# Kernel tuning notes

Hardware: AMD Instinct MI355X
Metric: run time of the kernel (lower is better)

The kernel has to match this reference:

```python
import jax, jax.numpy as jnp
import numpy as np

B, S, D, H = 4, 8192, 512, 8
HD = D // H  # head_dim = 64


def setup_inputs() -> dict:
    key0 = jax.random.key(0)
    ks = jax.random.split(key0, 8)
    scale_in = (2.0 / (D + 3 * D)) ** 0.5  # xavier_uniform-ish std
    scale_out = (2.0 / (D + D)) ** 0.5
    return {
        "query": jax.random.normal(ks[0], (B, S, D), dtype=jnp.float32),
        "key": jax.random.normal(ks[1], (B, S, D), dtype=jnp.float32),
        "value": jax.random.normal(ks[2], (B, S, D), dtype=jnp.float32),
        "key_padding_mask": jax.random.bernoulli(ks[3], 0.1, (B, S)),  # True = ignore
        "in_proj_weight": jax.random.normal(ks[4], (3 * D, D), dtype=jnp.float32) * scale_in,
        "in_proj_bias": jnp.zeros((3 * D,), dtype=jnp.float32),
        "out_proj_weight": jax.random.normal(ks[5], (D, D), dtype=jnp.float32) * scale_out,
        "out_proj_bias": jnp.zeros((D,), dtype=jnp.float32),
    }


def _phi(x):
    # ELU+1 feature map (strictly positive)
    return jax.nn.elu(x) + 1.0


def reference(query, key, value, key_padding_mask, in_proj_weight, in_proj_bias,
              out_proj_weight, out_proj_bias):
    # NB: the torch module projects q,k,v all from `query`; key/value args are unused.
    qkv = query @ in_proj_weight.T + in_proj_bias  # (B,S,3D)
    q, k, v = jnp.split(qkv, 3, axis=-1)
    # (B,S,D) -> (B,H,S,HD)
    def to_heads(x):
        return x.reshape(B, S, H, HD).transpose(0, 2, 1, 3)
    q = _phi(to_heads(q))
    k = _phi(to_heads(k))
    v = to_heads(v)
    mask = (~key_padding_mask).astype(q.dtype)[:, None, :, None]  # (B,1,S,1)
    k = k * mask
    v = v * mask
    kv = jnp.einsum('bhsd,bhse->bhde', k, v)          # (B,H,HD,HD)
    numerator = jnp.einsum('bhsd,bhde->bhse', q, kv)  # (B,H,S,HD)
    k_sum = k.sum(axis=2)                              # (B,H,HD)
    denominator = jnp.einsum('bhsd,bhd->bhs', q, k_sum)[..., None]
    denominator = jnp.maximum(denominator, 1e-6)
    attn_out = (numerator / denominator).transpose(0, 2, 1, 3).reshape(B, S, D)
    return attn_out @ out_proj_weight.T + out_proj_bias
```

## Files before the change

kernel.cpp:

```cpp
#include <hip/hip_runtime.h>
#include <cstddef>

#define B_   4
#define S_   8192
#define D_   512
#define H_   8
#define HD_  64
#define NROW (B_ * S_)
#define NQ   ((size_t)NROW * D_)

typedef __attribute__((ext_vector_type(4))) float  f32x4;
typedef __attribute__((ext_vector_type(8))) short  s16x8;
typedef __attribute__((ext_vector_type(4))) unsigned short u16x4;
typedef __attribute__((ext_vector_type(8))) unsigned short u16x8;

__device__ __forceinline__ float phi_f(float x) {
    return x > 0.0f ? x + 1.0f : expf(x);
}
__device__ __forceinline__ float bf2f(unsigned short u) {
    return __uint_as_float(((unsigned int)u) << 16);
}
__device__ __forceinline__ unsigned short f2bf(float f) {
    unsigned int u = __float_as_uint(f);
    u += 0x7fffu + ((u >> 16) & 1u);
    return (unsigned short)(u >> 16);
}

#define GLOBAL_AS(p) ((const __attribute__((address_space(1))) void*)(p))
#define LDS_AS(p)    ((__attribute__((address_space(3))) void*)(p))

__global__ void detect_mask(const unsigned char* __restrict__ m, int* __restrict__ flag) {
    __shared__ int sany;
    if (threadIdx.x == 0) sany = 0;
    __syncthreads();
    const uint4* mw = (const uint4*)m;
    unsigned int any = 0;
    #pragma unroll
    for (int r = 0; r < 8; ++r) {
        const uint4 w = mw[r * 256 + threadIdx.x];
        any |= (w.x | w.y | w.z | w.w) & 0xFFFFFF00u;
    }
    if (any) atomicOr(&sany, 1);
    __syncthreads();
    if (threadIdx.x == 0) *flag = sany ? 1 : 0;
}

__global__ __launch_bounds__(256) void convert_all(
    const float* __restrict__ q,  unsigned short* __restrict__ qb,
    const float* __restrict__ wi, unsigned short* __restrict__ wib,
    const float* __restrict__ wo, unsigned short* __restrict__ wob,
    const unsigned char* __restrict__ kpm, const int* __restrict__ flag,
    float* __restrict__ fmask)
{
    const size_t i = (size_t)blockIdx.x * 256 + threadIdx.x;
    {
        const float4 v = *(const float4*)&q[i * 4];
        u16x4 o; o.x = f2bf(v.x); o.y = f2bf(v.y); o.z = f2bf(v.z); o.w = f2bf(v.w);
        *(u16x4*)&qb[i * 4] = o;
    }
    if (i < 786432 / 4) {
        const float4 v = *(const float4*)&wi[i * 4];
        u16x4 o; o.x = f2bf(v.x); o.y = f2bf(v.y); o.z = f2bf(v.z); o.w = f2bf(v.w);
        *(u16x4*)&wib[i * 4] = o;
    }
    if (i < 262144 / 4) {
        const float4 v = *(const float4*)&wo[i * 4];
        u16x4 o; o.x = f2bf(v.x); o.y = f2bf(v.y); o.z = f2bf(v.z); o.w = f2bf(v.w);
        *(u16x4*)&wob[i * 4] = o;
    }
    if (i < NROW) {
        const bool ignore = (*flag) ? (kpm[i] != 0) : (((const int*)kpm)[i] != 0);
        fmask[i] = ignore ? 0.0f : 1.0f;
    }
}

__global__ __launch_bounds__(256) void gemm_mfma(
    const unsigned short* __restrict__ A,  int lda,
    const unsigned short* __restrict__ Bw, int ldb,
    const float* __restrict__ bias, int K, int mode,
    const float* __restrict__ fmask,
    unsigned short* __restrict__ Cq,
    unsigned short* __restrict__ Ck,
    unsigned short* __restrict__ Cv,
    float* __restrict__ Cout)
{
    __shared__ __align__(16) unsigned short As[3][128 * 32];
    __shared__ __align__(16) unsigned short Bs[3][128 * 32];
    __shared__ float fm[128];

    const int t    = threadIdx.x;
    const int lane = t & 63;
    const int wave = t >> 6;
    const int wm   = wave & 1;
    const int wn   = wave >> 1;

    const int nbx = gridDim.x;
    const int nwg = nbx * gridDim.y;
    int id = blockIdx.y * nbx + blockIdx.x;
    id = (id & 7) * (nwg >> 3) + (id >> 3);
    const int m0 = (id / nbx) * 128;
    const int n0 = (id % nbx) * 128;

    if (mode == 0 && t < 128) fm[t] = fmask[m0 + t];

    f32x4 acc[4][4] = {};

    const int sr  = lane >> 2;
    const int skc = (((lane & 3) ^ ((lane >> 3) & 3))) * 8;

    const int nt = K >> 5;

    #define STAGE(kt_, buf_)                                                            \
        do {                                                                            \
            const int k0_ = (kt_) << 5;                                                 \
            _Pragma("unroll")                                                           \
            for (int j = 0; j < 2; ++j) {                                               \
                const int row = wave * 32 + j * 16;                                     \
                const unsigned short* g = A + (size_t)(m0 + row + sr) * lda + k0_ + skc;\
                __builtin_amdgcn_global_load_lds(GLOBAL_AS(g),                          \
                    LDS_AS(&As[(buf_)][row * 32]), 16, 0, 0);                           \
            }                                                                           \
            _Pragma("unroll")                                                           \
            for (int j = 0; j < 2; ++j) {                                               \
                const int row = wave * 32 + j * 16;                                     \
                const unsigned short* g = Bw + (size_t)(n0 + row + sr) * ldb + k0_ + skc;\
                __builtin_amdgcn_global_load_lds(GLOBAL_AS(g),                          \
                    LDS_AS(&Bs[(buf_)][row * 32]), 16, 0, 0);                           \
            }                                                                           \
        } while (0)

    STAGE(0, 0);
    STAGE(1, 1);

    const int fr = lane & 15;
    const int cn = lane >> 4;
    const int fo = (cn ^ ((fr >> 1) & 3)) * 8;

    int cur = 0;
    for (int kt = 0; kt < nt; ++kt) {
        if (kt + 1 < nt) asm volatile("s_waitcnt vmcnt(4)" ::: "memory");
        else             asm volatile("s_waitcnt vmcnt(0)" ::: "memory");
        __builtin_amdgcn_s_barrier();

        if (kt + 2 < nt) {
            int nb = cur + 2; if (nb >= 3) nb -= 3;
            STAGE(kt + 2, nb);
        }

        s16x8 af[4], bf[4];
        #pragma unroll
        for (int i = 0; i < 4; ++i)
            af[i] = *(const s16x8*)&As[cur][(wm * 64 + i * 16 + fr) * 32 + fo];
        #pragma unroll
        for (int j = 0; j < 4; ++j)
            bf[j] = *(const s16x8*)&Bs[cur][(wn * 64 + j * 16 + fr) * 32 + fo];
        #pragma unroll
        for (int i = 0; i < 4; ++i)
            #pragma unroll
            for (int j = 0; j < 4; ++j)
                acc[i][j] = __builtin_amdgcn_mfma_f32_16x16x32_bf16(af[i], bf[j], acc[i][j], 0, 0, 0);

        if (++cur == 3) cur = 0;
    }
    #undef STAGE

    const int col  = lane & 15;
    const int rowq = (lane >> 4) * 4;
    float bj[4];
    #pragma unroll
    for (int j = 0; j < 4; ++j) bj[j] = bias[n0 + wn * 64 + j * 16 + col];

    if (mode == 1) {
        #pragma unroll
        for (int i = 0; i < 4; ++i)
            #pragma unroll
            for (int r = 0; r < 4; ++r) {
                const int m = m0 + wm * 64 + i * 16 + rowq + r;
                #pragma unroll
                for (int j = 0; j < 4; ++j) {
                    const int n = n0 + wn * 64 + j * 16 + col;
                    Cout[(size_t)m * D_ + n] = acc[i][j][r] + bj[j];
                }
            }
    } else {
        const int region = n0 >> 9;
        unsigned short* Cb = region == 0 ? Cq : (region == 1 ? Ck : Cv);
        #pragma unroll
        for (int i = 0; i < 4; ++i)
            #pragma unroll
            for (int r = 0; r < 4; ++r) {
                const int ml = wm * 64 + i * 16 + rowq + r;
                const int m  = m0 + ml;
                const float mk = fm[ml];
                #pragma unroll
                for (int j = 0; j < 4; ++j) {
                    const int n  = (n0 & 511) + wn * 64 + j * 16 + col;
                    float v = acc[i][j][r] + bj[j];
                    if (region == 0)      v = phi_f(v);
                    else if (region == 1) v = phi_f(v) * mk;
                    else                  v = v * mk;
                    Cb[(size_t)m * D_ + n] = f2bf(v);
                }
            }
    }
}

__global__ __launch_bounds__(256) void kv_reduce(
    const unsigned short* __restrict__ kbuf,
    const unsigned short* __restrict__ vbuf,
    float* __restrict__ part_kv,
    float* __restrict__ part_ks)
{
    const int bh = blockIdx.x, chunk = blockIdx.y;
    const int b = bh >> 3, h = bh & 7;

    __shared__ __align__(16) float Ks[16][68];
    __shared__ __align__(16) float Vs[16][68];

    const int t    = threadIdx.x;
    const int wave = t >> 6;
    const int lane = t & 63;
    const int tx   = lane & 7;
    const int ty   = lane >> 3;

    const int sr = (t & 127) >> 3;
    const int sc = (t & 7) * 8;
    const unsigned short* src = (t < 128 ? kbuf : vbuf) + (size_t)b * S_ * D_ + h * HD_;
    float (*dst)[68] = (t < 128) ? Ks : Vs;

    float acc[8][8] = {};
    float ks[8] = {};
    const int s0 = chunk * (S_ / 16);
    const int NIT = 32;

    u16x8 x = *(const u16x8*)&src[(size_t)(s0 + sr) * D_ + sc];

    for (int it = 0; it < NIT; ++it) {
        __syncthreads();
        float4 f0, f1;
        f0.x = bf2f(x[0]); f0.y = bf2f(x[1]); f0.z = bf2f(x[2]); f0.w = bf2f(x[3]);
        f1.x = bf2f(x[4]); f1.y = bf2f(x[5]); f1.z = bf2f(x[6]); f1.w = bf2f(x[7]);
        *(float4*)&dst[sr][sc]     = f0;
        *(float4*)&dst[sr][sc + 4] = f1;
        __syncthreads();
        u16x8 xn = {};
        if (it + 1 < NIT)
            xn = *(const u16x8*)&src[(size_t)(s0 + (it + 1) * 16 + sr) * D_ + sc];
        #pragma unroll
        for (int ss0 = 0; ss0 < 4; ++ss0) {
            const int ss = wave + ss0 * 4;
            const float4 a0 = *(const float4*)&Ks[ss][ty * 8];
            const float4 a1 = *(const float4*)&Ks[ss][ty * 8 + 4];
            const float4 v0 = *(const float4*)&Vs[ss][tx * 8];
            const float4 v1 = *(const float4*)&Vs[ss][tx * 8 + 4];
            const float av[8] = {a0.x, a0.y, a0.z, a0.w, a1.x, a1.y, a1.z, a1.w};
            const float vv[8] = {v0.x, v0.y, v0.z, v0.w, v1.x, v1.y, v1.z, v1.w};
            #pragma unroll
            for (int i2 = 0; i2 < 8; ++i2)
                #pragma unroll
                for (int j2 = 0; j2 < 8; ++j2)
                    acc[i2][j2] += av[i2] * vv[j2];
            if (tx == 0) {
                #pragma unroll
                for (int i2 = 0; i2 < 8; ++i2) ks[i2] += av[i2];
            }
        }
        x = xn;
    }

    const int p = bh * 64 + chunk * 4 + wave;
    float* pk = part_kv + (size_t)p * 4096;
    #pragma unroll
    for (int i2 = 0; i2 < 8; ++i2) {
        #pragma unroll
        for (int j4 = 0; j4 < 2; ++j4) {
            float4 o;
            o.x = acc[i2][j4 * 4 + 0]; o.y = acc[i2][j4 * 4 + 1];
            o.z = acc[i2][j4 * 4 + 2]; o.w = acc[i2][j4 * 4 + 3];
            *(float4*)&pk[(ty * 8 + i2) * 64 + tx * 8 + j4 * 4] = o;
        }
    }
    if (tx == 0) {
        float* ps = part_ks + (size_t)p * 64;
        #pragma unroll
        for (int i2 = 0; i2 < 8; ++i2) ps[ty * 8 + i2] = ks[i2];
    }
}

__global__ void kv_reduce2(const float* __restrict__ part_kv,
                           const float* __restrict__ part_ks,
                           unsigned short* __restrict__ kvT,
                           unsigned short* __restrict__ ksumb)
{
    const int i = blockIdx.x * 256 + threadIdx.x;
    if (i < 32 * 4096) {
        const int bh = i >> 12, de = i & 4095;
        const int d = de >> 6, e = de & 63;
        float s = 0.0f;
        #pragma unroll
        for (int c = 0; c < 64; ++c) s += part_kv[(size_t)(bh * 64 + c) * 4096 + de];
        kvT[bh * 4096 + e * 64 + d] = f2bf(s);
    }
    if (i < 32 * 64) {
        const int bh = i >> 6, e = i & 63;
        float s = 0.0f;
        #pragma unroll
        for (int c = 0; c < 64; ++c) s += part_ks[(size_t)(bh * 64 + c) * 64 + e];
        ksumb[i] = f2bf(s);
    }
}

__global__ __launch_bounds__(256) void apply_attn_mfma(
    const unsigned short* __restrict__ qphi,
    const unsigned short* __restrict__ kvT,
    const unsigned short* __restrict__ ksumb,
    unsigned short* __restrict__ attnb)
{
    const int bh = blockIdx.x;
    const int b  = bh >> 3, h = bh & 7;
    const int m0 = blockIdx.y * 128;

    const int t    = threadIdx.x;
    const int lane = t & 63;
    const int wave = t >> 6;
    const int fr   = lane & 15;
    const int fk   = (lane >> 4) * 8;
    const int row0 = m0 + wave * 32;

    const unsigned short* Ah = qphi + (size_t)(b * S_ + row0) * D_ + h * HD_;
    const unsigned short* Bh = kvT + bh * 4096;
    const unsigned short* Kh = ksumb + bh * 64;

    s16x8 af[2][2], bfr[2][4], bd[2];
    #pragma unroll
    for (int kc = 0; kc < 2; ++kc) {
        #pragma unroll
        for (int i = 0; i < 2; ++i)
            af[kc][i] = *(const s16x8*)&Ah[(size_t)(i * 16 + fr) * D_ + kc * 32 + fk];
        #pragma unroll
        for (int j = 0; j < 4; ++j)
            bfr[kc][j] = *(const s16x8*)&Bh[(j * 16 + fr) * 64 + kc * 32 + fk];
        bd[kc] = *(const s16x8*)&Kh[kc * 32 + fk];
    }

    f32x4 acc[2][4] = {};
    f32x4 accd[2] = {};
    #pragma unroll
    for (int kc = 0; kc < 2; ++kc)
        #pragma unroll
        for (int i = 0; i < 2; ++i) {
            #pragma unroll
            for (int j = 0; j < 4; ++j)
                acc[i][j] = __builtin_amdgcn_mfma_f32_16x16x32_bf16(af[kc][i], bfr[kc][j], acc[i][j], 0, 0, 0);
            accd[i] = __builtin_amdgcn_mfma_f32_16x16x32_bf16(af[kc][i], bd[kc], accd[i], 0, 0, 0);
        }

    const int rq = (lane >> 4) * 4;
    #pragma unroll
    for (int i = 0; i < 2; ++i)
        #pragma unroll
        for (int r = 0; r < 4; ++r) {
            const float inv = 1.0f / fmaxf(accd[i][r], 1e-6f);
            const size_t row = (size_t)(b * S_ + row0 + i * 16 + rq + r);
            #pragma unroll
            for (int j = 0; j < 4; ++j)
                attnb[row * D_ + h * HD_ + j * 16 + fr] = f2bf(acc[i][j][r] * inv);
        }
}

extern "C" void kernel_launch(void* const* d_in, const int* in_sizes, int n_in,
                              void* d_out, int out_size, void* d_ws, size_t ws_size,
                              hipStream_t stream)
{
    const float* query       = (const float*)d_in[0];
    const unsigned char* kpm = (const unsigned char*)d_in[3];
    const float* w_in        = (const float*)d_in[4];
    const float* b_in        = (const float*)d_in[5];
    const float* w_out       = (const float*)d_in[6];
    const float* b_out       = (const float*)d_in[7];
    float* out = (float*)d_out;

    unsigned short* qb    = (unsigned short*)d_ws;
    unsigned short* qphi  = qb    + NQ;
    unsigned short* kpb   = qphi  + NQ;
    unsigned short* vmb   = kpb   + NQ;
    unsigned short* wib   = vmb   + NQ;
    unsigned short* wob   = wib   + 1536 * 512;
    float* fmask   = (float*)(wob + 512 * 512);
    float* part_kv = fmask + NROW;
    float* part_ks = part_kv + (size_t)2048 * 4096;
    unsigned short* kvTb  = (unsigned short*)(part_ks + 2048 * 64);
    unsigned short* ksumb = kvTb + 32 * 4096;
    int*   flag    = (int*)(ksumb + 32 * 64);

    hipLaunchKernelGGL(detect_mask, dim3(1), dim3(256), 0, stream, kpm, flag);
    hipLaunchKernelGGL(convert_all, dim3(16384), dim3(256), 0, stream,
                       query, qb, w_in, wib, w_out, wob, kpm, flag, fmask);

    hipLaunchKernelGGL(gemm_mfma, dim3(1536 / 128, NROW / 128), dim3(256), 0, stream,
                       qb, D_, wib, D_, b_in, D_, 0, fmask,
                       qphi, kpb, vmb, (float*)nullptr);

    hipLaunchKernelGGL(kv_reduce, dim3(32, 16), dim3(256), 0, stream, kpb, vmb, part_kv, part_ks);
    hipLaunchKernelGGL(kv_reduce2, dim3(512), dim3(256), 0, stream,
                       part_kv, part_ks, kvTb, ksumb);

    hipLaunchKernelGGL(apply_attn_mfma, dim3(32, S_ / 128), dim3(256), 0, stream,
                       qphi, kvTb, ksumb, qb);

    hipLaunchKernelGGL(gemm_mfma, dim3(512 / 128, NROW / 128), dim3(256), 0, stream,
                       qb, D_, wob, D_, b_out, D_, 1, (const float*)nullptr,
                       (unsigned short*)nullptr, (unsigned short*)nullptr,
                       (unsigned short*)nullptr, out);
}
```

Baseline: 386.1 us.

## Enlarge GEMM tile to 256x128 and switch to double-buffered LDS pipeline

The shared MFMA GEMM kernel now computes a 256x128 output tile per workgroup. Each wave owns 64 rows across all 128 columns, so it issues 32 MFMAs per k-step against 8 shared B fragments. The three-stage prefetch with vmcnt waits is replaced by a simpler two-buffer scheme using __syncthreads at each step, and the grid is halved in M. The aim is more reuse of B per loaded tile and fewer workgroups, at the cost of more accumulator registers (128 floats per thread), lower occupancy, and a shallower prefetch pipeline.

New measurement: 467.3 us. +21.0%, slower.

```diff
diff --git a/kernel.cpp b/kernel.cpp
--- a/kernel.cpp
+++ b/kernel.cpp
@@ -84,26 +84,24 @@
     unsigned short* __restrict__ Cv,
     float* __restrict__ Cout)
 {
-    __shared__ __align__(16) unsigned short As[3][128 * 32];
-    __shared__ __align__(16) unsigned short Bs[3][128 * 32];
-    __shared__ float fm[128];
+    __shared__ __align__(16) unsigned short As[2][256 * 32];
+    __shared__ __align__(16) unsigned short Bs[2][128 * 32];
+    __shared__ float fm[256];
 
     const int t    = threadIdx.x;
     const int lane = t & 63;
     const int wave = t >> 6;
-    const int wm   = wave & 1;
-    const int wn   = wave >> 1;
 
     const int nbx = gridDim.x;
     const int nwg = nbx * gridDim.y;
     int id = blockIdx.y * nbx + blockIdx.x;
     id = (id & 7) * (nwg >> 3) + (id >> 3);
-    const int m0 = (id / nbx) * 128;
+    const int m0 = (id / nbx) * 256;
     const int n0 = (id % nbx) * 128;
 
-    if (mode == 0 && t < 128) fm[t] = fmask[m0 + t];
-
-    f32x4 acc[4][4] = {};
+    if (mode == 0) fm[t] = fmask[m0 + t];
+
+    f32x4 acc[4][8] = {};
 
     const int sr  = lane >> 2;
     const int skc = (((lane & 3) ^ ((lane >> 3) & 3))) * 8;
@@ -114,14 +112,14 @@
         do {                                                                            \
             const int k0_ = (kt_) << 5;                                                 \
             _Pragma("unroll")                                                           \
-            for (int j = 0; j < 2; ++j) {                                               \
-                const int row = wave * 32 + j * 16;                                     \
+            for (int j = 0; j < 4; ++j) {              \
+                const int row = wave * 64 + j * 16;                                     \
                 const unsigned short* g = A + (size_t)(m0 + row + sr) * lda + k0_ + skc;\
                 __builtin_amdgcn_global_load_lds(GLOBAL_AS(g),                          \
                     LDS_AS(&As[(buf_)][row * 32]), 16, 0, 0);                           \
             }                                                                           \
             _Pragma("unroll")                                                           \
-            for (int j = 0; j < 2; ++j) {                                               \
+            for (int j = 0; j < 2; ++j) {              \
                 const int row = wave * 32 + j * 16;                                     \
                 const unsigned short* g = Bw + (size_t)(n0 + row + sr) * ldb + k0_ + skc;\
                 __builtin_amdgcn_global_load_lds(GLOBAL_AS(g),                          \
@@ -130,55 +128,48 @@
         } while (0)
 
     STAGE(0, 0);
-    STAGE(1, 1);
+    __syncthreads();
 
     const int fr = lane & 15;
     const int cn = lane >> 4;
     const int fo = (cn ^ ((fr >> 1) & 3)) * 8;
 
-    int cur = 0;
     for (int kt = 0; kt < nt; ++kt) {
-        if (kt + 1 < nt) asm volatile("s_waitcnt vmcnt(4)" ::: "memory");
-        else             asm volatile("s_waitcnt vmcnt(0)" ::: "memory");
-        __builtin_amdgcn_s_barrier();
-
-        if (kt + 2 < nt) {
-            int nb = cur + 2; if (nb >= 3) nb -= 3;
-            STAGE(kt + 2, nb);
-        }
-
-        s16x8 af[4], bf[4];
+        const int cur = kt & 1;
+        if (kt + 1 < nt) STAGE(kt + 1, cur ^ 1);
+
+        s16x8 af[4], bf[8];
         #pragma unroll
         for (int i = 0; i < 4; ++i)
-            af[i] = *(const s16x8*)&As[cur][(wm * 64 + i * 16 + fr) * 32 + fo];
-        #pragma unroll
-        for (int j = 0; j < 4; ++j)
-            bf[j] = *(const s16x8*)&Bs[cur][(wn * 64 + j * 16 + fr) * 32 + fo];
+            af[i] = *(const s16x8*)&As[cur][(wave * 64 + i * 16 + fr) * 32 + fo];
+        #pragma unroll
+        for (int j = 0; j < 8; ++j)
+            bf[j] = *(const s16x8*)&Bs[cur][(j * 16 + fr) * 32 + fo];
         #pragma unroll
         for (int i = 0; i < 4; ++i)
             #pragma unroll
-            for (int j = 0; j < 4; ++j)
+            for (int j = 0; j < 8; ++j)
                 acc[i][j] = __builtin_amdgcn_mfma_f32_16x16x32_bf16(af[i], bf[j], acc[i][j], 0, 0, 0);
 
-        if (++cur == 3) cur = 0;
+        __syncthreads();
     }
     #undef STAGE
 
-    const int col  = lane & 15;
+    const int colf = lane & 15;
     const int rowq = (lane >> 4) * 4;
-    float bj[4];
-    #pragma unroll
-    for (int j = 0; j < 4; ++j) bj[j] = bias[n0 + wn * 64 + j * 16 + col];
+    float bj[8];
+    #pragma unroll
+    for (int j = 0; j < 8; ++j) bj[j] = bias[n0 + j * 16 + colf];
 
     if (mode == 1) {
         #pragma unroll
         for (int i = 0; i < 4; ++i)
             #pragma unroll
             for (int r = 0; r < 4; ++r) {
-                const int m = m0 + wm * 64 + i * 16 + rowq + r;
+                const int m = m0 + wave * 64 + i * 16 + rowq + r;
                 #pragma unroll
-                for (int j = 0; j < 4; ++j) {
-                    const int n = n0 + wn * 64 + j * 16 + col;
+                for (int j = 0; j < 8; ++j) {
+                    const int n = n0 + j * 16 + colf;
                     Cout[(size_t)m * D_ + n] = acc[i][j][r] + bj[j];
                 }
             }
@@ -189,12 +180,12 @@
         for (int i = 0; i < 4; ++i)
             #pragma unroll
             for (int r = 0; r < 4; ++r) {
-                const int ml = wm * 64 + i * 16 + rowq + r;
+                const int ml = wave * 64 + i * 16 + rowq + r;
                 const int m  = m0 + ml;
                 const float mk = fm[ml];
                 #pragma unroll
-                for (int j = 0; j < 4; ++j) {
-                    const int n  = (n0 & 511) + wn * 64 + j * 16 + col;
+                for (int j = 0; j < 8; ++j) {
+                    const int n  = (n0 & 511) + j * 16 + colf;
                     float v = acc[i][j][r] + bj[j];
                     if (region == 0)      v = phi_f(v);
                     else if (region == 1) v = phi_f(v) * mk;
@@ -397,7 +388,7 @@
     hipLaunchKernelGGL(convert_all, dim3(16384), dim3(256), 0, stream,
                        query, qb, w_in, wib, w_out, wob, kpm, flag, fmask);
 
-    hipLaunchKernelGGL(gemm_mfma, dim3(1536 / 128, NROW / 128), dim3(256), 0, stream,
+    hipLaunchKernelGGL(gemm_mfma, dim3(1536 / 128, NROW / 256), dim3(256), 0, stream,
                        qb, D_, wib, D_, b_in, D_, 0, fmask,
                        qphi, kpb, vmb, (float*)nullptr);
 
@@ -408,7 +399,7 @@
     hipLaunchKernelGGL(apply_attn_mfma, dim3(32, S_ / 128), dim3(256), 0, stream,
                        qphi, kvTb, ksumb, qb);
 
-    hipLaunchKernelGGL(gemm_mfma, dim3(512 / 128, NROW / 128), dim3(256), 0, stream,
+    hipLaunchKernelGGL(gemm_mfma, dim3(512 / 128, NROW / 256), dim3(256), 0, stream,
                        qb, D_, wob, D_, b_out, D_, 1, (const float*)nullptr,
                        (unsigned short*)nullptr, (unsigned short*)nullptr,
                        (unsigned short*)nullptr, out);
```

## Fuse attention application with output projection via LDS-resident tile

Applied to the files above, without the earlier changes.

Replaces the separate attention-apply kernel and the output-projection GEMM with one kernel. Each 512-thread block computes a 64-row attention tile for all 8 heads, normalises it, and keeps it in shared memory as bf16. It then multiplies that tile by the output weight, streaming the weight through double-buffered LDS with global_load_lds. This removes the bf16 attention round trip through global memory and one launch. In exchange each block re-reads the full 512x512 weight, uses about 130KB of LDS, which limits occupancy, and runs a serialised per-k-step barrier pipeline.

Result: no change. 387.6 us (+0.4%).

```diff
diff --git a/kernel.cpp b/kernel.cpp
--- a/kernel.cpp
+++ b/kernel.cpp
@@ -310,61 +310,125 @@
     }
 }
 
-__global__ __launch_bounds__(256) void apply_attn_mfma(
+__global__ __launch_bounds__(512) void attn_outproj(
     const unsigned short* __restrict__ qphi,
     const unsigned short* __restrict__ kvT,
     const unsigned short* __restrict__ ksumb,
-    unsigned short* __restrict__ attnb)
-{
-    const int bh = blockIdx.x;
-    const int b  = bh >> 3, h = bh & 7;
-    const int m0 = blockIdx.y * 128;
+    const unsigned short* __restrict__ wo,
+    const float* __restrict__ bias,
+    float* __restrict__ out)
+{
+    __shared__ __align__(16) unsigned short An[64][520];
+    __shared__ __align__(16) unsigned short Bs[2][512 * 32];
 
     const int t    = threadIdx.x;
     const int lane = t & 63;
-    const int wave = t >> 6;
-    const int fr   = lane & 15;
-    const int fk   = (lane >> 4) * 8;
-    const int row0 = m0 + wave * 32;
-
-    const unsigned short* Ah = qphi + (size_t)(b * S_ + row0) * D_ + h * HD_;
-    const unsigned short* Bh = kvT + bh * 4096;
-    const unsigned short* Kh = ksumb + bh * 64;
-
-    s16x8 af[2][2], bfr[2][4], bd[2];
+    const int wv   = t >> 6;
+    const int r0   = blockIdx.x * 64;
+    const int b    = r0 >> 13;
+    const int bh   = b * 8 + wv;
+
+    const int fr = lane & 15;
+    const int fk = (lane >> 4) * 8;
+    const int rq = (lane >> 4) * 4;
+
+    {
+        const unsigned short* Ah = qphi + (size_t)r0 * D_ + wv * HD_;
+        const unsigned short* Bh = kvT + bh * 4096;
+        const unsigned short* Kh = ksumb + bh * 64;
+
+        s16x8 af[2][4], bfr[2][4], bd[2];
+        #pragma unroll
+        for (int kc = 0; kc < 2; ++kc) {
+            #pragma unroll
+            for (int i = 0; i < 4; ++i)
+                af[kc][i] = *(const s16x8*)&Ah[(size_t)(i * 16 + fr) * D_ + kc * 32 + fk];
+            #pragma unroll
+            for (int j = 0; j < 4; ++j)
+                bfr[kc][j] = *(const s16x8*)&Bh[(j * 16 + fr) * 64 + kc * 32 + fk];
+            bd[kc] = *(const s16x8*)&Kh[kc * 32 + fk];
+        }
+
+        f32x4 acc[4][4] = {};
+        f32x4 accd[4] = {};
+        #pragma unroll
+        for (int kc = 0; kc < 2; ++kc)
+            #pragma unroll
+            for (int i = 0; i < 4; ++i) {
+                #pragma unroll
+                for (int j = 0; j < 4; ++j)
+                    acc[i][j] = __builtin_amdgcn_mfma_f32_16x16x32_bf16(af[kc][i], bfr[kc][j], acc[i][j], 0, 0, 0);
+                accd[i] = __builtin_amdgcn_mfma_f32_16x16x32_bf16(af[kc][i], bd[kc], accd[i], 0, 0, 0);
+            }
+
+        #pragma unroll
+        for (int i = 0; i < 4; ++i)
+            #pragma unroll
+            for (int r = 0; r < 4; ++r) {
+                const float inv = 1.0f / fmaxf(accd[i][r], 1e-6f);
+                const int row = i * 16 + rq + r;
+                #pragma unroll
+                for (int j = 0; j < 4; ++j)
+                    An[row][wv * 64 + j * 16 + fr] = f2bf(acc[i][j][r] * inv);
+            }
+    }
+
+    const int sr  = lane >> 2;
+    const int skc = (((lane & 3) ^ ((lane >> 3) & 3))) * 8;
+    const int cn  = lane >> 4;
+    const int fo  = (cn ^ ((fr >> 1) & 3)) * 8;
+
+    #define WSTAGE(kt_, buf_)                                                           \
+        do {                                                                            \
+            _Pragma("unroll")                                                           \
+            for (int j = 0; j < 4; ++j) {              \
+                const int row = wv * 64 + j * 16;                                       \
+                const unsigned short* g = wo + (size_t)(row + sr) * D_ + ((kt_) << 5) + skc;\
+                __builtin_amdgcn_global_load_lds(GLOBAL_AS(g),                          \
+                    LDS_AS(&Bs[(buf_)][row * 32]), 16, 0, 0);                           \
+            }                                                                           \
+        } while (0)
+
+    WSTAGE(0, 0);
+    __syncthreads();
+
+    const int wm2 = wv >> 2;
+    const int wn4 = wv & 3;
+    f32x4 acc2[2][8] = {};
+
+    for (int kt = 0; kt < 16; ++kt) {
+        const int cur = kt & 1;
+        if (kt + 1 < 16) WSTAGE(kt + 1, cur ^ 1);
+
+        s16x8 a2[2], b2[8];
+        #pragma unroll
+        for (int i = 0; i < 2; ++i)
+            a2[i] = *(const s16x8*)&An[wm2 * 32 + i * 16 + fr][kt * 32 + fk];
+        #pragma unroll
+        for (int j = 0; j < 8; ++j)
+            b2[j] = *(const s16x8*)&Bs[cur][(wn4 * 128 + j * 16 + fr) * 32 + fo];
+        #pragma unroll
+        for (int i = 0; i < 2; ++i)
+            #pragma unroll
+            for (int j = 0; j < 8; ++j)
+                acc2[i][j] = __builtin_amdgcn_mfma_f32_16x16x32_bf16(a2[i], b2[j], acc2[i][j], 0, 0, 0);
+
+        __syncthreads();
+    }
+    #undef WSTAGE
+
+    float bj[8];
     #pragma unroll
-    for (int kc = 0; kc < 2; ++kc) {
-        #pragma unroll
-        for (int i = 0; i < 2; ++i)
-            af[kc][i] = *(const s16x8*)&Ah[(size_t)(i * 16 + fr) * D_ + kc * 32 + fk];
-        #pragma unroll
-        for (int j = 0; j < 4; ++j)
-            bfr[kc][j] = *(const s16x8*)&Bh[(j * 16 + fr) * 64 + kc * 32 + fk];
-        bd[kc] = *(const s16x8*)&Kh[kc * 32 + fk];
-    }
-
-    f32x4 acc[2][4] = {};
-    f32x4 accd[2] = {};
-    #pragma unroll
-    for (int kc = 0; kc < 2; ++kc)
-        #pragma unroll
-        for (int i = 0; i < 2; ++i) {
-            #pragma unroll
-            for (int j = 0; j < 4; ++j)
-                acc[i][j] = __builtin_amdgcn_mfma_f32_16x16x32_bf16(af[kc][i], bfr[kc][j], acc[i][j], 0, 0, 0);
-            accd[i] = __builtin_amdgcn_mfma_f32_16x16x32_bf16(af[kc][i], bd[kc], accd[i], 0, 0, 0);
-        }
-
-    const int rq = (lane >> 4) * 4;
+    for (int j = 0; j < 8; ++j) bj[j] = bias[wn4 * 128 + j * 16 + fr];
+
     #pragma unroll
     for (int i = 0; i < 2; ++i)
         #pragma unroll
         for (int r = 0; r < 4; ++r) {
-            const float inv = 1.0f / fmaxf(accd[i][r], 1e-6f);
-            const size_t row = (size_t)(b * S_ + row0 + i * 16 + rq + r);
-            #pragma unroll
-            for (int j = 0; j < 4; ++j)
-                attnb[row * D_ + h * HD_ + j * 16 + fr] = f2bf(acc[i][j][r] * inv);
+            const int m = r0 + wm2 * 32 + i * 16 + rq + r;
+            #pragma unroll
+            for (int j = 0; j < 8; ++j)
+                out[(size_t)m * D_ + wn4 * 128 + j * 16 + fr] = acc2[i][j][r] + bj[j];
         }
 }
 
@@ -405,11 +469,6 @@
     hipLaunchKernelGGL(kv_reduce2, dim3(512), dim3(256), 0, stream,
                        part_kv, part_ks, kvTb, ksumb);
 
-    hipLaunchKernelGGL(apply_attn_mfma, dim3(32, S_ / 128), dim3(256), 0, stream,
-                       qphi, kvTb, ksumb, qb);
-
-    hipLaunchKernelGGL(gemm_mfma, dim3(512 / 128, NROW / 128), dim3(256), 0, stream,
-                       qb, D_, wob, D_, b_out, D_, 1, (const float*)nullptr,
-                       (unsigned short*)nullptr, (unsigned short*)nullptr,
-                       (unsigned short*)nullptr, out);
-}
+    hipLaunchKernelGGL(attn_outproj, dim3(NROW / 64), dim3(512), 0, stream,
+                       qphi, kvTb, ksumb, wob, b_out, out);
+}
```
